# Kernel tuning notes

Hardware: AMD Instinct MI355X
Metric: run time of the kernel (lower is better)

## Reference

```python
import jax, jax.numpy as jnp
import numpy as np

SEQ_LEN = 8192
VOCAB = 128000
EMB = 10   # embedding_size hard-coded in RNNLM.__init__
HID = 10   # hidden_size hard-coded


def setup_inputs() -> dict:
    key = jax.random.key(0)
    k1, k2, k3, k4, k5, k6 = jax.random.split(key, 6)
    input_batch = jax.random.randint(k1, (SEQ_LEN, 1), 0, VOCAB, dtype=jnp.int32)
    embedding = jax.random.normal(k2, (VOCAB, EMB), dtype=jnp.float32)
    # nn.Linear(input+hidden -> hidden) and nn.Linear(input+hidden -> vocab)
    W_i2h = jax.random.normal(k3, (HID, EMB + HID), dtype=jnp.float32) * 0.1
    b_i2h = jax.random.normal(k4, (HID,), dtype=jnp.float32) * 0.1
    W_i2o = jax.random.normal(k5, (VOCAB, EMB + HID), dtype=jnp.float32) * 0.1
    b_i2o = jax.random.normal(k6, (VOCAB,), dtype=jnp.float32) * 0.1
    return {
        "input_batch": input_batch,
        "embedding": embedding,
        "W_i2h": W_i2h,
        "b_i2h": b_i2h,
        "W_i2o": W_i2o,
        "b_i2o": b_i2o,
    }


def reference(input_batch, embedding, W_i2h, b_i2h, W_i2o, b_i2o):
    # Elman RNN unrolled over time via lax.scan; batch is 1 (required by the
    # original torch.cat of [B,10] embedding with [1,10] hidden state).
    def step(hidden, word_ix):
        w = embedding[word_ix]                              # (1, EMB)
        combined = jnp.concatenate([w, hidden], axis=1)     # (1, EMB+HID)
        new_hidden = combined @ W_i2h.T + b_i2h             # (1, HID)
        logits = combined @ W_i2o.T + b_i2o                 # (1, VOCAB)
        logp = jax.nn.log_softmax(logits, axis=1)
        pred = jnp.argmax(logp, axis=1).astype(jnp.float32)  # topk(1) index
        return new_hidden, pred

    hidden0 = jnp.zeros((1, HID), dtype=jnp.float32)
    _, preds = jax.lax.scan(step, hidden0, input_batch)     # preds: (SEQ_LEN, 1)
    return preds
```

## Files before the change

kernel.cpp:

```cpp
#include <hip/hip_runtime.h>

#define SEQ   8192
#define VOCAB 128000
#define L     64
#define NCH   128

#define OFF_CMB    0
#define OFF_CVEC   163840
#define OFF_AMAX   245760
#define OFF_AMAX1  262144
#define OFF_CNORM  270336
#define OFF_WPART  278528
#define OFF_WMAX   279040
#define OFF_C32    279104
#define OFF_W32    410176

#define TBLK   16
#define VSL2   125
#define VSPAN  1024
#define NIT    32
#define SEEDTB 32
#define SEEDSL 32
#define CCAP   4096

typedef __attribute__((ext_vector_type(8))) short bf16x8;
typedef __attribute__((ext_vector_type(4))) float f32x4;

static __device__ inline unsigned short f2bf(float x) {
    unsigned u = __float_as_uint(x);
    u += 0x7FFF + ((u >> 16) & 1);
    return (unsigned short)(u >> 16);
}
static __device__ inline unsigned sortable(float x) {
    unsigned u = __float_as_uint(x);
    return (u & 0x80000000u) ? ~u : (u | 0x80000000u);
}
static __device__ inline float unsortable(unsigned k) {
    unsigned u = (k & 0x80000000u) ? (k & 0x7FFFFFFFu) : ~k;
    return __uint_as_float(u);
}

__global__ void k_prep(const int* __restrict__ ix, const float* __restrict__ emb,
                       const float* __restrict__ Wih, const float* __restrict__ bih,
                       const float* __restrict__ Wio, const float* __restrict__ bio,
                       float* __restrict__ ws) {
    int b = blockIdx.x;
    int tid = threadIdx.x;
    if (b < 32) {
        int t = b * 256 + tid;
        ((unsigned long long*)(ws + OFF_AMAX))[t] = 0ULL;
        ((unsigned*)(ws + OFF_AMAX1))[t] = 0u;

        int id = ix[t];
        float w[10];
        const float2* ep = (const float2*)(emb + (long long)id * 10);
#pragma unroll
        for (int j = 0; j < 5; j++) ((float2*)w)[j] = ep[j];
#pragma unroll
        for (int j = 0; j < 10; j++) ws[OFF_CMB + j * SEQ + t] = w[j];

        int m = t >> 6, k = t & 63;
        float* cv = ws + OFF_CVEC + (k * NCH + m) * 10;
#pragma unroll
        for (int i = 0; i < 10; i++) {
            float s = bih[i];
#pragma unroll
            for (int j = 0; j < 10; j++) s += Wih[i * 20 + j] * w[j];
            cv[i] = s;
        }
    } else {
        __shared__ float red[4];
        int bs = b - 32;
        int v = bs * 256 + tid;
        float w[20];
        const float4* r = (const float4*)(Wio + (long long)v * 20);
#pragma unroll
        for (int q = 0; q < 5; q++) ((float4*)w)[q] = r[q];
        float bv = bio[v];
        float n2 = bv * bv;
#pragma unroll
        for (int k = 0; k < 20; k++) n2 += w[k] * w[k];
        float nrm = sqrtf(n2);
        for (int off = 1; off < 64; off <<= 1)
            nrm = fmaxf(nrm, __shfl_xor(nrm, off));
        if ((tid & 63) == 0) red[tid >> 6] = nrm;
        __syncthreads();
        if (tid == 0)
            ws[OFF_WPART + bs] = fmaxf(fmaxf(red[0], red[1]), fmaxf(red[2], red[3]));

        unsigned short h[32];
#pragma unroll
        for (int k = 0; k < 20; k++) h[k] = f2bf(w[k]);
        h[20] = f2bf(bv);
#pragma unroll
        for (int k = 21; k < 32; k++) h[k] = 0;
        uint4* dst = (uint4*)((unsigned short*)(ws + OFF_W32));
#pragma unroll
        for (int i = 0; i < 4; i++) {
            uint4 u;
            u.x = (unsigned)h[8*i+0] | ((unsigned)h[8*i+1] << 16);
            u.y = (unsigned)h[8*i+2] | ((unsigned)h[8*i+3] << 16);
            u.z = (unsigned)h[8*i+4] | ((unsigned)h[8*i+5] << 16);
            u.w = (unsigned)h[8*i+6] | ((unsigned)h[8*i+7] << 16);
            dst[v * 4 + i] = u;
        }
    }
}

__global__ void k_scan(const float* __restrict__ Wih, float* __restrict__ ws) {
    __shared__ float P[100], Q[100];
    __shared__ float Dl[NCH][10];
    __shared__ float Hst[NCH][10];
    __shared__ float Hl[10];
    int tid = threadIdx.x;

    float Ar[10][10];
#pragma unroll
    for (int i = 0; i < 10; i++)
#pragma unroll
        for (int j = 0; j < 10; j++) Ar[i][j] = Wih[i * 20 + 10 + j];

    {
        int m = tid;
        float h[10];
#pragma unroll
        for (int i = 0; i < 10; i++) h[i] = 0.f;
        const float* cvb = ws + OFF_CVEC;
        float2 buf[5];
        {
            const float2* cp = (const float2*)(cvb + m * 10);
#pragma unroll
            for (int j = 0; j < 5; j++) buf[j] = cp[j];
        }
        for (int k = 0; k < L; k++) {
            float cc[10];
#pragma unroll
            for (int j = 0; j < 5; j++) { cc[2*j] = buf[j].x; cc[2*j+1] = buf[j].y; }
            if (k + 1 < L) {
                const float2* cp = (const float2*)(cvb + ((k + 1) * NCH + m) * 10);
#pragma unroll
                for (int j = 0; j < 5; j++) buf[j] = cp[j];
            }
            float nh[10];
#pragma unroll
            for (int i = 0; i < 10; i++) {
                float s = cc[i];
#pragma unroll
                for (int j = 0; j < 10; j++) s += Ar[i][j] * h[j];
                nh[i] = s;
            }
#pragma unroll
            for (int i = 0; i < 10; i++) h[i] = nh[i];
        }
#pragma unroll
        for (int i = 0; i < 10; i++) Dl[m][i] = h[i];
    }

    if (tid < 100) P[tid] = Wih[(tid / 10) * 20 + 10 + (tid % 10)];
    __syncthreads();
    for (int it = 0; it < 6; it++) {
        if (tid < 100) {
            int i = tid / 10, j = tid % 10;
            float s = 0.f;
#pragma unroll
            for (int k = 0; k < 10; k++) s += P[i * 10 + k] * P[k * 10 + j];
            Q[tid] = s;
        }
        __syncthreads();
        if (tid < 100) P[tid] = Q[tid];
        __syncthreads();
    }

    if (tid < 10) Hl[tid] = 0.f;
    __syncthreads();
    if (tid < 10) {
        int i = tid;
        float a64[10];
#pragma unroll
        for (int j = 0; j < 10; j++) a64[j] = P[i * 10 + j];
        float hc = 0.f;
        for (int m = 0; m < NCH; m++) {
            Hst[m][i] = hc;
            float s = Dl[m][i];
#pragma unroll
            for (int j = 0; j < 10; j++) s += a64[j] * Hl[j];
            Hl[i] = s;
            hc = s;
        }
    }
    __syncthreads();

    {
        int m = tid;
        float h[10];
#pragma unroll
        for (int i = 0; i < 10; i++) h[i] = Hst[m][i];
        const float* cvb = ws + OFF_CVEC;
        float2 buf[5];
        {
            const float2* cp = (const float2*)(cvb + m * 10);
#pragma unroll
            for (int j = 0; j < 5; j++) buf[j] = cp[j];
        }
        for (int k = 0; k < L; k++) {
            int tg = m * 64 + k;
            float cc[10];
#pragma unroll
            for (int j = 0; j < 5; j++) { cc[2*j] = buf[j].x; cc[2*j+1] = buf[j].y; }
            if (k + 1 < L) {
                const float2* cp = (const float2*)(cvb + ((k + 1) * NCH + m) * 10);
#pragma unroll
                for (int j = 0; j < 5; j++) buf[j] = cp[j];
            }
#pragma unroll
            for (int i = 0; i < 10; i++) ws[OFF_CMB + (10 + i) * SEQ + tg] = h[i];
            float nh[10];
#pragma unroll
            for (int i = 0; i < 10; i++) {
                float s = cc[i];
#pragma unroll
                for (int j = 0; j < 10; j++) s += Ar[i][j] * h[j];
                nh[i] = s;
            }
#pragma unroll
            for (int i = 0; i < 10; i++) h[i] = nh[i];
        }
    }
}

__global__ void k_pack_c(float* __restrict__ ws) {
    int b = blockIdx.x;
    int tid = threadIdx.x;
    if (b == 32) {
        __shared__ float red[4];
        float m = 0.f;
        for (int i = tid; i < 500; i += 256) m = fmaxf(m, ws[OFF_WPART + i]);
        for (int off = 1; off < 64; off <<= 1)
            m = fmaxf(m, __shfl_xor(m, off));
        if ((tid & 63) == 0) red[tid >> 6] = m;
        __syncthreads();
        if (tid == 0)
            ws[OFF_WMAX] = fmaxf(fmaxf(red[0], red[1]), fmaxf(red[2], red[3]));
        return;
    }
    int t = b * 256 + tid;
    float c[20];
#pragma unroll
    for (int k = 0; k < 20; k++) c[k] = ws[OFF_CMB + k * SEQ + t];
    float n2 = 1.0f;
#pragma unroll
    for (int k = 0; k < 20; k++) n2 += c[k] * c[k];
    ws[OFF_CNORM + t] = sqrtf(n2);

    unsigned short h[32];
#pragma unroll
    for (int k = 0; k < 20; k++) h[k] = f2bf(c[k]);
    h[20] = f2bf(1.0f);
#pragma unroll
    for (int k = 21; k < 32; k++) h[k] = 0;
    uint4* dst = (uint4*)((unsigned short*)(ws + OFF_C32));
#pragma unroll
    for (int i = 0; i < 4; i++) {
        uint4 u;
        u.x = (unsigned)h[8*i+0] | ((unsigned)h[8*i+1] << 16);
        u.y = (unsigned)h[8*i+2] | ((unsigned)h[8*i+3] << 16);
        u.z = (unsigned)h[8*i+4] | ((unsigned)h[8*i+5] << 16);
        u.w = (unsigned)h[8*i+6] | ((unsigned)h[8*i+7] << 16);
        dst[t * 4 + i] = u;
    }
}

__global__ __launch_bounds__(256, 4)
void k_seed(const float* __restrict__ ws, unsigned* __restrict__ amax1) {
    int tid = threadIdx.x;
    int lane = tid & 63, wid = tid >> 6, quad = lane >> 4, col = lane & 15;
    int tb  = blockIdx.x >> 5;
    int sl  = blockIdx.x & 31;
    int t0w = tb * 256 + wid * 64;
    int v0s = sl * VSPAN;

    const unsigned short* c32 = (const unsigned short*)(ws + OFF_C32);
    const unsigned short* Wg  = (const unsigned short*)(ws + OFF_W32);

    bf16x8 a[4];
#pragma unroll
    for (int tt = 0; tt < 4; tt++)
        a[tt] = *(const bf16x8*)(c32 + (t0w + tt * 16 + col) * 32 + quad * 8);

    const f32x4 zero = {0.f, 0.f, 0.f, 0.f};
    float run[4][4];
#pragma unroll
    for (int tt = 0; tt < 4; tt++)
#pragma unroll
        for (int g = 0; g < 4; g++) run[tt][g] = -3.4e38f;

    const unsigned short* Wb = Wg + (unsigned)(v0s + col) * 32 + quad * 8;
    bf16x8 nb0 = *(const bf16x8*)(Wb);
    bf16x8 nb1 = *(const bf16x8*)(Wb + 512);

    for (int p = 0; p < NIT; ++p) {
        bf16x8 b0 = nb0, b1 = nb1;
        int pn = (p + 1 < NIT) ? p + 1 : p;
        const unsigned short* Wn = Wb + pn * 1024;
        nb0 = *(const bf16x8*)(Wn);
        nb1 = *(const bf16x8*)(Wn + 512);
#pragma unroll
        for (int tt = 0; tt < 4; tt++) {
            f32x4 d0 = __builtin_amdgcn_mfma_f32_16x16x32_bf16(a[tt], b0, zero, 0, 0, 0);
            f32x4 d1 = __builtin_amdgcn_mfma_f32_16x16x32_bf16(a[tt], b1, zero, 0, 0, 0);
#pragma unroll
            for (int g = 0; g < 4; g++)
                run[tt][g] = fmaxf(run[tt][g], fmaxf(d0[g], d1[g]));
        }
    }

#pragma unroll
    for (int tt = 0; tt < 4; tt++)
#pragma unroll
        for (int g = 0; g < 4; g++) {
            float r = run[tt][g];
            for (int off = 1; off < 16; off <<= 1)
                r = fmaxf(r, __shfl_xor(r, off));
            if (col == 0)
                atomicMax(&amax1[t0w + tt * 16 + quad * 4 + g], sortable(r));
        }
}

__global__ __launch_bounds__(256, 4)
void k_cand(const float* __restrict__ ws, const float* __restrict__ Wio,
            const float* __restrict__ bio, const unsigned* __restrict__ amax1,
            unsigned long long* __restrict__ amax) {
    __shared__ unsigned cand[CCAP];
    __shared__ unsigned cnt;

    int tid = threadIdx.x;
    int lane = tid & 63, wid = tid >> 6, quad = lane >> 4, col = lane & 15;
    int tb  = blockIdx.x & 15;
    int sl  = blockIdx.x >> 4;
    int t0w = tb * 512 + wid * 128;
    int v0s = sl * VSPAN;
    if (tid == 0) cnt = 0;
    __syncthreads();

    const unsigned short* c32 = (const unsigned short*)(ws + OFF_C32);
    const unsigned short* Wg  = (const unsigned short*)(ws + OFF_W32);
    float wmax = ws[OFF_WMAX];

    bf16x8 a[8];
    float thr[8][4];
#pragma unroll
    for (int tt = 0; tt < 8; tt++) {
        a[tt] = *(const bf16x8*)(c32 + (t0w + tt * 16 + col) * 32 + quad * 8);
#pragma unroll
        for (int g = 0; g < 4; g++) {
            int t = t0w + tt * 16 + quad * 4 + g;
            float maxap = unsortable(amax1[t]);
            thr[tt][g] = maxap - (0.04f * ws[OFF_CNORM + t] * wmax + 1e-5f);
        }
    }

    const f32x4 zero = {0.f, 0.f, 0.f, 0.f};
    const unsigned short* Wb = Wg + (unsigned)(v0s + col) * 32 + quad * 8;
    bf16x8 nb0 = *(const bf16x8*)(Wb);
    bf16x8 nb1 = *(const bf16x8*)(Wb + 512);

    unsigned mask[8];
#pragma unroll
    for (int tt = 0; tt < 8; tt++) mask[tt] = 0u;

    for (int p = 0; p < NIT; ++p) {
        bf16x8 b0 = nb0, b1 = nb1;
        int pn = (p + 1 < NIT) ? p + 1 : p;
        const unsigned short* Wn = Wb + pn * 1024;
        nb0 = *(const bf16x8*)(Wn);
        nb1 = *(const bf16x8*)(Wn + 512);
        unsigned bit = 1u << p;
#pragma unroll
        for (int tt = 0; tt < 8; tt++) {
            f32x4 d0 = __builtin_amdgcn_mfma_f32_16x16x32_bf16(a[tt], b0, zero, 0, 0, 0);
            f32x4 d1 = __builtin_amdgcn_mfma_f32_16x16x32_bf16(a[tt], b1, zero, 0, 0, 0);
            unsigned hit = 0u;
#pragma unroll
            for (int g = 0; g < 4; g++) {
                float mg = fmaxf(d0[g], d1[g]);
                hit |= (mg >= thr[tt][g]) ? bit : 0u;
            }
            mask[tt] |= hit;
        }
    }

#pragma unroll
    for (int tt = 0; tt < 8; tt++) {
        unsigned m = mask[tt];
        for (int off = 1; off < 64; off <<= 1)
            m |= __shfl_xor(m, off);
        while (m) {
            int p = __ffs(m) - 1;
            m &= m - 1;
            const unsigned short* Wp = Wb + p * 1024;
            bf16x8 b0 = *(const bf16x8*)(Wp);
            bf16x8 b1 = *(const bf16x8*)(Wp + 512);
            f32x4 d0 = __builtin_amdgcn_mfma_f32_16x16x32_bf16(a[tt], b0, zero, 0, 0, 0);
            f32x4 d1 = __builtin_amdgcn_mfma_f32_16x16x32_bf16(a[tt], b1, zero, 0, 0, 0);
            int v0 = v0s + p * 32 + col;
#pragma unroll
            for (int g = 0; g < 4; g++) {
                unsigned t = (unsigned)(t0w + tt * 16 + quad * 4 + g);
                if (d0[g] >= thr[tt][g]) {
                    unsigned idx = atomicAdd(&cnt, 1u);
                    if (idx < CCAP) cand[idx] = (t << 17) | (unsigned)v0;
                }
                if (d1[g] >= thr[tt][g]) {
                    unsigned idx = atomicAdd(&cnt, 1u);
                    if (idx < CCAP) cand[idx] = (t << 17) | (unsigned)(v0 + 16);
                }
            }
        }
    }

    __syncthreads();
    unsigned n = cnt < CCAP ? cnt : CCAP;
    const float* cmb = ws + OFF_CMB;
    for (unsigned i = tid; i < n; i += 256) {
        unsigned e = cand[i];
        int t = (int)(e >> 17);
        int v = (int)(e & 0x1FFFFu);
        const float* wr = Wio + (long long)v * 20;
        float ex = bio[v];
#pragma unroll
        for (int k = 0; k < 20; k++)
            ex = fmaf(wr[k], cmb[k * SEQ + t], ex);
        unsigned key = sortable(ex);
        unsigned long long packed =
            ((unsigned long long)key << 32) | (unsigned)(VOCAB - v);
        unsigned long long cur = amax[t];
        if (packed > cur)
            atomicMax(&amax[t], packed);
    }
}

__global__ void k_out(const unsigned long long* __restrict__ amax,
                      float* __restrict__ out) {
    int t = blockIdx.x * blockDim.x + threadIdx.x;
    if (t >= SEQ) return;
    unsigned long long p = amax[t];
    int idx = VOCAB - (int)(p & 0xFFFFFFFFu);
    out[t] = (float)idx;
}

extern "C" void kernel_launch(void* const* d_in, const int* in_sizes, int n_in,
                              void* d_out, int out_size, void* d_ws, size_t ws_size,
                              hipStream_t stream) {
    (void)in_sizes; (void)n_in; (void)out_size; (void)ws_size;
    const int*   ix  = (const int*)d_in[0];
    const float* emb = (const float*)d_in[1];
    const float* Wih = (const float*)d_in[2];
    const float* bih = (const float*)d_in[3];
    const float* Wio = (const float*)d_in[4];
    const float* bio = (const float*)d_in[5];
    float* out = (float*)d_out;
    float* ws  = (float*)d_ws;
    unsigned long long* amax = (unsigned long long*)(ws + OFF_AMAX);
    unsigned* amax1 = (unsigned*)(ws + OFF_AMAX1);

    hipLaunchKernelGGL(k_prep,   dim3(532),             dim3(256), 0, stream, ix, emb, Wih, bih, Wio, bio, ws);
    hipLaunchKernelGGL(k_scan,   dim3(1),               dim3(128), 0, stream, Wih, ws);
    hipLaunchKernelGGL(k_pack_c, dim3(33),              dim3(256), 0, stream, ws);
    hipLaunchKernelGGL(k_seed,   dim3(SEEDTB * SEEDSL), dim3(256), 0, stream, ws, amax1);
    hipLaunchKernelGGL(k_cand,   dim3(TBLK * VSL2),     dim3(256), 0, stream, ws, Wio, bio, amax1, amax);
    hipLaunchKernelGGL(k_out,    dim3(SEQ / 256),       dim3(256), 0, stream, amax, out);
}
```

Baseline: 300.6 us.

## Retile candidate kernel with wave-level max filter and XCD-aware block mapping

```diff
diff --git a/kernel.cpp b/kernel.cpp
--- a/kernel.cpp
+++ b/kernel.cpp
@@ -15,13 +15,15 @@
 #define OFF_C32    279104
 #define OFF_W32    410176
 
-#define TBLK   16
-#define VSL2   125
-#define VSPAN  1024
-#define NIT    32
-#define SEEDTB 32
-#define SEEDSL 32
-#define CCAP   4096
+#define CTB    32
+#define CSL    160
+#define CVSPAN 800
+#define CNIT   25
+#define STB    32
+#define SSL    32
+#define SVSPAN 1024
+#define SNIT   32
+#define CCAP   2048
 
 typedef __attribute__((ext_vector_type(8))) short bf16x8;
 typedef __attribute__((ext_vector_type(4))) float f32x4;
@@ -274,10 +276,12 @@
 void k_seed(const float* __restrict__ ws, unsigned* __restrict__ amax1) {
     int tid = threadIdx.x;
     int lane = tid & 63, wid = tid >> 6, quad = lane >> 4, col = lane & 15;
-    int tb  = blockIdx.x >> 5;
-    int sl  = blockIdx.x & 31;
+    int r  = blockIdx.x & 7;
+    int q  = blockIdx.x >> 3;
+    int tb = q & 31;
+    int sl = (q >> 5) * 8 + r;
     int t0w = tb * 256 + wid * 64;
-    int v0s = sl * VSPAN;
+    int v0s = sl * SVSPAN;
 
     const unsigned short* c32 = (const unsigned short*)(ws + OFF_C32);
     const unsigned short* Wg  = (const unsigned short*)(ws + OFF_W32);
@@ -298,9 +302,9 @@
     bf16x8 nb0 = *(const bf16x8*)(Wb);
     bf16x8 nb1 = *(const bf16x8*)(Wb + 512);
 
-    for (int p = 0; p < NIT; ++p) {
+    for (int p = 0; p < SNIT; ++p) {
         bf16x8 b0 = nb0, b1 = nb1;
-        int pn = (p + 1 < NIT) ? p + 1 : p;
+        int pn = (p + 1 < SNIT) ? p + 1 : p;
         const unsigned short* Wn = Wb + pn * 1024;
         nb0 = *(const bf16x8*)(Wn);
         nb1 = *(const bf16x8*)(Wn + 512);
@@ -318,15 +322,15 @@
     for (int tt = 0; tt < 4; tt++)
 #pragma unroll
         for (int g = 0; g < 4; g++) {
-            float r = run[tt][g];
+            float r2 = run[tt][g];
             for (int off = 1; off < 16; off <<= 1)
-                r = fmaxf(r, __shfl_xor(r, off));
+                r2 = fmaxf(r2, __shfl_xor(r2, off));
             if (col == 0)
-                atomicMax(&amax1[t0w + tt * 16 + quad * 4 + g], sortable(r));
-        }
-}
-
-__global__ __launch_bounds__(256, 4)
+                atomicMax(&amax1[t0w + tt * 16 + quad * 4 + g], sortable(r2));
+        }
+}
+
+__global__ __launch_bounds__(256, 8)
 void k_cand(const float* __restrict__ ws, const float* __restrict__ Wio,
             const float* __restrict__ bio, const unsigned* __restrict__ amax1,
             unsigned long long* __restrict__ amax) {
@@ -335,10 +339,12 @@
 
     int tid = threadIdx.x;
     int lane = tid & 63, wid = tid >> 6, quad = lane >> 4, col = lane & 15;
-    int tb  = blockIdx.x & 15;
-    int sl  = blockIdx.x >> 4;
-    int t0w = tb * 512 + wid * 128;
-    int v0s = sl * VSPAN;
+    int r  = blockIdx.x & 7;
+    int q  = blockIdx.x >> 3;
+    int tb = q & 31;
+    int sl = (q >> 5) * 8 + r;
+    int t0w = tb * 256 + wid * 64;
+    int v0s = sl * CVSPAN;
     if (tid == 0) cnt = 0;
     __syncthreads();
 
@@ -346,16 +352,17 @@
     const unsigned short* Wg  = (const unsigned short*)(ws + OFF_W32);
     float wmax = ws[OFF_WMAX];
 
-    bf16x8 a[8];
-    float thr[8][4];
-#pragma unroll
-    for (int tt = 0; tt < 8; tt++) {
+    bf16x8 a[4];
+    float thrmin = 3.4e38f;
+#pragma unroll
+    for (int tt = 0; tt < 4; tt++) {
         a[tt] = *(const bf16x8*)(c32 + (t0w + tt * 16 + col) * 32 + quad * 8);
 #pragma unroll
         for (int g = 0; g < 4; g++) {
             int t = t0w + tt * 16 + quad * 4 + g;
-            float maxap = unsortable(amax1[t]);
-            thr[tt][g] = maxap - (0.04f * ws[OFF_CNORM + t] * wmax + 1e-5f);
+            float thr = unsortable(amax1[t]) -
+                        (0.04f * ws[OFF_CNORM + t] * wmax + 1e-5f);
+            thrmin = fminf(thrmin, thr);
         }
     }
 
@@ -364,34 +371,29 @@
     bf16x8 nb0 = *(const bf16x8*)(Wb);
     bf16x8 nb1 = *(const bf16x8*)(Wb + 512);
 
-    unsigned mask[8];
-#pragma unroll
-    for (int tt = 0; tt < 8; tt++) mask[tt] = 0u;
-
-    for (int p = 0; p < NIT; ++p) {
+    unsigned mask = 0u;
+
+    for (int p = 0; p < CNIT; ++p) {
         bf16x8 b0 = nb0, b1 = nb1;
-        int pn = (p + 1 < NIT) ? p + 1 : p;
+        int pn = (p + 1 < CNIT) ? p + 1 : p;
         const unsigned short* Wn = Wb + pn * 1024;
         nb0 = *(const bf16x8*)(Wn);
         nb1 = *(const bf16x8*)(Wn + 512);
-        unsigned bit = 1u << p;
-#pragma unroll
-        for (int tt = 0; tt < 8; tt++) {
+        float hmax = -3.4e38f;
+#pragma unroll
+        for (int tt = 0; tt < 4; tt++) {
             f32x4 d0 = __builtin_amdgcn_mfma_f32_16x16x32_bf16(a[tt], b0, zero, 0, 0, 0);
             f32x4 d1 = __builtin_amdgcn_mfma_f32_16x16x32_bf16(a[tt], b1, zero, 0, 0, 0);
-            unsigned hit = 0u;
-#pragma unroll
-            for (int g = 0; g < 4; g++) {
-                float mg = fmaxf(d0[g], d1[g]);
-                hit |= (mg >= thr[tt][g]) ? bit : 0u;
-            }
-            mask[tt] |= hit;
-        }
-    }
-
-#pragma unroll
-    for (int tt = 0; tt < 8; tt++) {
-        unsigned m = mask[tt];
+            float q0 = fmaxf(fmaxf(d0[0], d0[1]), d0[2]);
+            float q1 = fmaxf(fmaxf(d0[3], d1[0]), d1[1]);
+            float q2 = fmaxf(fmaxf(d1[2], d1[3]), q0);
+            hmax = fmaxf(hmax, fmaxf(q1, q2));
+        }
+        mask |= (hmax >= thrmin) ? (1u << p) : 0u;
+    }
+
+    {
+        unsigned m = mask;
         for (int off = 1; off < 64; off <<= 1)
             m |= __shfl_xor(m, off);
         while (m) {
@@ -400,19 +402,24 @@
             const unsigned short* Wp = Wb + p * 1024;
             bf16x8 b0 = *(const bf16x8*)(Wp);
             bf16x8 b1 = *(const bf16x8*)(Wp + 512);
-            f32x4 d0 = __builtin_amdgcn_mfma_f32_16x16x32_bf16(a[tt], b0, zero, 0, 0, 0);
-            f32x4 d1 = __builtin_amdgcn_mfma_f32_16x16x32_bf16(a[tt], b1, zero, 0, 0, 0);
             int v0 = v0s + p * 32 + col;
 #pragma unroll
-            for (int g = 0; g < 4; g++) {
-                unsigned t = (unsigned)(t0w + tt * 16 + quad * 4 + g);
-                if (d0[g] >= thr[tt][g]) {
-                    unsigned idx = atomicAdd(&cnt, 1u);
-                    if (idx < CCAP) cand[idx] = (t << 17) | (unsigned)v0;
-                }
-                if (d1[g] >= thr[tt][g]) {
-                    unsigned idx = atomicAdd(&cnt, 1u);
-                    if (idx < CCAP) cand[idx] = (t << 17) | (unsigned)(v0 + 16);
+            for (int tt = 0; tt < 4; tt++) {
+                f32x4 d0 = __builtin_amdgcn_mfma_f32_16x16x32_bf16(a[tt], b0, zero, 0, 0, 0);
+                f32x4 d1 = __builtin_amdgcn_mfma_f32_16x16x32_bf16(a[tt], b1, zero, 0, 0, 0);
+#pragma unroll
+                for (int g = 0; g < 4; g++) {
+                    int t = t0w + tt * 16 + quad * 4 + g;
+                    float thr = unsortable(amax1[t]) -
+                                (0.04f * ws[OFF_CNORM + t] * wmax + 1e-5f);
+                    if (d0[g] >= thr) {
+                        unsigned idx = atomicAdd(&cnt, 1u);
+                        if (idx < CCAP) cand[idx] = ((unsigned)t << 17) | (unsigned)v0;
+                    }
+                    if (d1[g] >= thr) {
+                        unsigned idx = atomicAdd(&cnt, 1u);
+                        if (idx < CCAP) cand[idx] = ((unsigned)t << 17) | (unsigned)(v0 + 16);
+                    }
                 }
             }
         }
@@ -463,10 +470,10 @@
     unsigned long long* amax = (unsigned long long*)(ws + OFF_AMAX);
     unsigned* amax1 = (unsigned*)(ws + OFF_AMAX1);
 
-    hipLaunchKernelGGL(k_prep,   dim3(532),             dim3(256), 0, stream, ix, emb, Wih, bih, Wio, bio, ws);
-    hipLaunchKernelGGL(k_scan,   dim3(1),               dim3(128), 0, stream, Wih, ws);
-    hipLaunchKernelGGL(k_pack_c, dim3(33),              dim3(256), 0, stream, ws);
-    hipLaunchKernelGGL(k_seed,   dim3(SEEDTB * SEEDSL), dim3(256), 0, stream, ws, amax1);
-    hipLaunchKernelGGL(k_cand,   dim3(TBLK * VSL2),     dim3(256), 0, stream, ws, Wio, bio, amax1, amax);
-    hipLaunchKernelGGL(k_out,    dim3(SEQ / 256),       dim3(256), 0, stream, amax, out);
-}
+    hipLaunchKernelGGL(k_prep,   dim3(532),       dim3(256), 0, stream, ix, emb, Wih, bih, Wio, bio, ws);
+    hipLaunchKernelGGL(k_scan,   dim3(1),         dim3(128), 0, stream, Wih, ws);
+    hipLaunchKernelGGL(k_pack_c, dim3(33),        dim3(256), 0, stream, ws);
+    hipLaunchKernelGGL(k_seed,   dim3(STB * SSL), dim3(256), 0, stream, ws, amax1);
+    hipLaunchKernelGGL(k_cand,   dim3(CTB * CSL), dim3(256), 0, stream, ws, Wio, bio, amax1, amax);
+    hipLaunchKernelGGL(k_out,    dim3(SEQ / 256), dim3(256), 0, stream, amax, out);
+}
```

Result: slower. 342.9 us (+14.1%).
